# Performance work log

Hardware: AMD Instinct MI355X
Metric: run time of the kernel (lower is better)

Reference implementation:

```python
import jax, jax.numpy as jnp
import numpy as np

N_NODES = 100000
N_EDGES = 1600000
D_IN, D_HID, D_OUT = 64, 64, 32


def _glorot(key, shape):
    fan_in, fan_out = shape[0], shape[1]
    lim = np.sqrt(6.0 / (fan_in + fan_out)).astype(np.float32)
    return jax.random.uniform(key, shape, jnp.float32, -lim, lim)


def setup_inputs() -> dict:
    key = jax.random.key(0)
    ks = jax.random.split(key, 12)
    x = jax.random.normal(ks[0], (N_NODES, D_IN), jnp.float32)
    edge_index = jax.random.randint(ks[1], (2, N_EDGES), 0, N_NODES, jnp.int64)
    return {
        "x": x,
        "edge_index": edge_index,
        # SAGEConv 1 (in->hid): lin_l (aggregated neighbors, with bias), lin_r (root, no bias)
        "Wl1": _glorot(ks[2], (D_IN, D_HID)),
        "Wr1": _glorot(ks[3], (D_IN, D_HID)),
        "b1": jnp.zeros((D_HID,), jnp.float32),
        # SAGEConv 2 (hid->out)
        "Wl2": _glorot(ks[4], (D_HID, D_OUT)),
        "Wr2": _glorot(ks[5], (D_HID, D_OUT)),
        "b2": jnp.zeros((D_OUT,), jnp.float32),
        # trust head: Linear(32,16) -> ReLU -> Linear(16,1) -> Sigmoid (dropout inert in eval)
        "Wt1": _glorot(ks[6], (D_OUT, 16)),
        "bt1": jnp.zeros((16,), jnp.float32),
        "Wt2": _glorot(ks[7], (16, 1)),
        "bt2": jnp.zeros((1,), jnp.float32),
    }


def _sage_conv(x, src, dst, Wl, Wr, b):
    # mean-aggregate neighbor messages: msg flows src -> dst
    msg = x[src]                                              # [E, d] gather
    agg_sum = jax.ops.segment_sum(msg, dst, num_segments=N_NODES)
    deg = jax.ops.segment_sum(jnp.ones((src.shape[0],), x.dtype), dst,
                              num_segments=N_NODES)
    agg = agg_sum / jnp.maximum(deg, 1.0)[:, None]            # zero-degree -> 0
    return agg @ Wl + x @ Wr + b


def reference(x, edge_index, Wl1, Wr1, b1, Wl2, Wr2, b2, Wt1, bt1, Wt2, bt2):
    src, dst = edge_index[0], edge_index[1]
    h = _sage_conv(x, src, dst, Wl1, Wr1, b1)
    h = jax.nn.relu(h)                    # dropout p=0.3 inert in eval
    h = _sage_conv(h, src, dst, Wl2, Wr2, b2)
    t = jax.nn.relu(h @ Wt1 + bt1)        # dropout p=0.2 inert in eval
    trust = jax.nn.sigmoid(t @ Wt2 + bt2)
    return h, trust
```

## Files before the change

### kernel.cpp

```cpp
#include <hip/hip_runtime.h>
#include <math.h>


#define BCAP    9216
#define BKCHUNK 4096

__device__ inline unsigned short f2bf(float x) {
    unsigned u = __float_as_uint(x);
    unsigned r = u + 0x7fffu + ((u >> 16) & 1u);
    return (unsigned short)(r >> 16);
}
__device__ inline unsigned pack2(float a, float b) {
    return (unsigned)f2bf(a) | ((unsigned)f2bf(b) << 16);
}
__device__ inline float bflo(unsigned u) { return __uint_as_float(u << 16); }
__device__ inline float bfhi(unsigned u) { return __uint_as_float(u & 0xffff0000u); }

__global__ __launch_bounds__(256) void k_m1(
    const float* __restrict__ x,
    const float* __restrict__ Wl1, const float* __restrict__ Wr1,
    const float* __restrict__ b1,
    unsigned* __restrict__ u16b, float* __restrict__ v,
    const int* __restrict__ src, const int* __restrict__ dst,
    int* __restrict__ gcnt, unsigned* __restrict__ pairs,
    int N, int E, int nbuck, int GB)
{
    __shared__ __align__(16) char smem[50176];
    int tid = threadIdx.x;

    if ((int)blockIdx.x >= GB) {
        int* hist = (int*)smem;
        int e0 = ((int)blockIdx.x - GB) * BKCHUNK;
        int e1 = min(e0 + BKCHUNK, E);

        hist[tid] = 0;
        __syncthreads();
        for (int e = e0 + tid; e < e1; e += 256)
            atomicAdd(&hist[((unsigned)dst[e]) >> 9], 1);
        __syncthreads();
        if (tid < nbuck && hist[tid] > 0)
            hist[tid] = tid * BCAP + atomicAdd(&gcnt[tid], hist[tid]);
        __syncthreads();
        for (int e = e0 + tid; e < e1; e += 256) {
            int t = dst[e];
            int b = ((unsigned)t) >> 9;
            int pos = atomicAdd(&hist[b], 1);
            pairs[pos] = (unsigned)src[e] | ((unsigned)(t & 511) << 17);
        }
        return;
    }

    float* sXT = (float*)smem;
    float* sW  = (float*)(smem + 17408);
    int nblk = blockIdx.x * 64;

    for (int i = tid * 4; i < 64 * 64; i += 1024) {
        int r = i >> 6, c = i & 63;
        int node = nblk + r;
        float4 xv = (node < N) ? *(const float4*)&x[(size_t)node * 64 + c]
                               : make_float4(0.f, 0.f, 0.f, 0.f);
        sXT[(c + 0) * 68 + r] = xv.x;
        sXT[(c + 1) * 68 + r] = xv.y;
        sXT[(c + 2) * 68 + r] = xv.z;
        sXT[(c + 3) * 68 + r] = xv.w;
    }
    for (int i = tid * 4; i < 64 * 128; i += 1024) {
        int k = i >> 7, n = i & 127;
        const float* Wsrc = (n < 64) ? (Wl1 + k * 64 + n) : (Wr1 + k * 64 + (n - 64));
        *(float4*)&sW[k * 128 + n] = *(const float4*)Wsrc;
    }
    __syncthreads();

    int mg = tid >> 4, ng = tid & 15;
    int m0 = mg * 4, n0 = ng * 8;

    float acc[4][8];
    #pragma unroll
    for (int mi = 0; mi < 4; ++mi)
        #pragma unroll
        for (int ni = 0; ni < 8; ++ni) acc[mi][ni] = 0.0f;

    #pragma unroll 8
    for (int k = 0; k < 64; ++k) {
        float4 a  = *(float4*)&sXT[k * 68 + m0];
        float4 w0 = *(float4*)&sW[k * 128 + n0];
        float4 w1 = *(float4*)&sW[k * 128 + n0 + 4];
        float av[4] = {a.x, a.y, a.z, a.w};
        float wv[8] = {w0.x, w0.y, w0.z, w0.w, w1.x, w1.y, w1.z, w1.w};
        #pragma unroll
        for (int mi = 0; mi < 4; ++mi)
            #pragma unroll
            for (int ni = 0; ni < 8; ++ni)
                acc[mi][ni] = fmaf(av[mi], wv[ni], acc[mi][ni]);
    }

    bool isV = (n0 >= 64);
    if (isV) {
        float4 b0 = *(const float4*)&b1[n0 - 64];
        float4 b4 = *(const float4*)&b1[n0 - 64 + 4];
        float bb[8] = {b0.x, b0.y, b0.z, b0.w, b4.x, b4.y, b4.z, b4.w};
        #pragma unroll
        for (int mi = 0; mi < 4; ++mi) {
            int node = nblk + m0 + mi;
            if (node >= N) continue;
            float* dstp = &v[(size_t)node * 64 + (n0 - 64)];
            *(float4*)&dstp[0] = make_float4(acc[mi][0]+bb[0], acc[mi][1]+bb[1],
                                             acc[mi][2]+bb[2], acc[mi][3]+bb[3]);
            *(float4*)&dstp[4] = make_float4(acc[mi][4]+bb[4], acc[mi][5]+bb[5],
                                             acc[mi][6]+bb[6], acc[mi][7]+bb[7]);
        }
    } else {
        #pragma unroll
        for (int mi = 0; mi < 4; ++mi) {
            int node = nblk + m0 + mi;
            if (node >= N) continue;
            uint4 pk;
            pk.x = pack2(acc[mi][0], acc[mi][1]);
            pk.y = pack2(acc[mi][2], acc[mi][3]);
            pk.z = pack2(acc[mi][4], acc[mi][5]);
            pk.w = pack2(acc[mi][6], acc[mi][7]);
            *(uint4*)&u16b[(size_t)node * 32 + (n0 >> 1)] = pk;
        }
    }
}

__global__ __launch_bounds__(512) void k_csr(
    const unsigned* __restrict__ pairs, const int* __restrict__ gcnt,
    int2* __restrict__ nodeOff, int* __restrict__ adj, int N)
{
    __shared__ int hist[512];
    __shared__ int waveSum[8];
    int b = blockIdx.x;
    int tid = threadIdx.x;
    int count = min(gcnt[b], BCAP);
    const unsigned* pp = pairs + (size_t)b * BCAP;
    int base = b * BCAP;

    hist[tid] = 0;
    __syncthreads();
    for (int j = tid; j < count; j += 512)
        atomicAdd(&hist[pp[j] >> 17], 1);
    __syncthreads();

    int deg = hist[tid];
    int lane = tid & 63, wid = tid >> 6;
    int incl = deg;
    #pragma unroll
    for (int off = 1; off < 64; off <<= 1) {
        int t = __shfl_up(incl, off);
        if (lane >= off) incl += t;
    }
    if (lane == 63) waveSum[wid] = incl;
    __syncthreads();
    if (wid == 0 && lane < 8) {
        int s = waveSum[lane], orig = s;
        #pragma unroll
        for (int off = 1; off < 8; off <<= 1) {
            int t = __shfl_up(s, off);
            if (lane >= off) s += t;
        }
        waveSum[lane] = s - orig;
    }
    __syncthreads();
    int excl = incl - deg + waveSum[wid];

    int node = b * 512 + tid;
    if (node < N) nodeOff[node] = make_int2(base + excl, deg);
    __syncthreads();
    hist[tid] = excl;
    __syncthreads();

    for (int j = tid; j < count; j += 512) {
        unsigned e = pp[j];
        int pos = atomicAdd(&hist[e >> 17], 1);
        adj[base + pos] = (int)(e & 0x1FFFFu);
    }
}

__global__ __launch_bounds__(512) void k_m2(
    const int2* __restrict__ nodeOff, const int* __restrict__ adj,
    const unsigned* __restrict__ u16b, const float* __restrict__ v,
    const float* __restrict__ Wl2, const float* __restrict__ Wr2,
    const float* __restrict__ b2,
    unsigned* __restrict__ P16b, float* __restrict__ Qout, int N)
{
    __shared__ float sH[64 * 66];
    __shared__ float sW[64 * 64];
    int tid = threadIdx.x;
    int nodeBase = blockIdx.x * 64;

    for (int i = tid * 4; i < 64 * 64; i += 2048) {
        int k = i >> 6, n = i & 63;
        const float* Wsrc = (n < 32) ? (Wl2 + k * 32 + n) : (Wr2 + k * 32 + (n - 32));
        *(float4*)&sW[k * 64 + n] = *(const float4*)Wsrc;
    }

    int hw = tid >> 5;
    int lane = tid & 31;
    #pragma unroll
    for (int r = 0; r < 4; ++r) {
        int nLoc = hw * 4 + r;
        int n = nodeBase + nLoc;
        float h0 = 0.0f, h1v = 0.0f;
        if (n < N) {
            int2 od = nodeOff[n];
            int beg = od.x, end = od.x + od.y;
            float lo0=0.f,hi0=0.f,lo1=0.f,hi1=0.f,lo2=0.f,hi2=0.f,lo3=0.f,hi3=0.f;
            int i = beg;
            for (; i + 4 <= end; i += 4) {
                int s0 = adj[i], s1 = adj[i+1], s2 = adj[i+2], s3 = adj[i+3];
                unsigned w0 = u16b[(size_t)s0 * 32 + lane];
                unsigned w1 = u16b[(size_t)s1 * 32 + lane];
                unsigned w2 = u16b[(size_t)s2 * 32 + lane];
                unsigned w3 = u16b[(size_t)s3 * 32 + lane];
                lo0 += bflo(w0); hi0 += bfhi(w0);
                lo1 += bflo(w1); hi1 += bfhi(w1);
                lo2 += bflo(w2); hi2 += bfhi(w2);
                lo3 += bflo(w3); hi3 += bfhi(w3);
            }
            for (; i < end; ++i) {
                unsigned w = u16b[(size_t)adj[i] * 32 + lane];
                lo0 += bflo(w); hi0 += bfhi(w);
            }
            float mlo = (lo0 + lo1) + (lo2 + lo3);
            float mhi = (hi0 + hi1) + (hi2 + hi3);
            float invd = (od.y > 0) ? 1.0f / (float)od.y : 1.0f;
            float2 vv = ((const float2*)v)[(size_t)n * 32 + lane];
            h0  = fmaxf(mlo * invd + vv.x, 0.0f);
            h1v = fmaxf(mhi * invd + vv.y, 0.0f);
        }
        *(float2*)&sH[nLoc * 66 + 2 * lane] = make_float2(h0, h1v);
    }
    __syncthreads();

    int ng = tid & 15;
    int mg = tid >> 4;
    int m0 = mg * 2, n0 = ng * 4;

    float acc[2][4];
    #pragma unroll
    for (int mi = 0; mi < 2; ++mi)
        #pragma unroll
        for (int ni = 0; ni < 4; ++ni) acc[mi][ni] = 0.0f;

    #pragma unroll 8
    for (int k = 0; k < 64; ++k) {
        float a0 = sH[(m0 + 0) * 66 + k];
        float a1 = sH[(m0 + 1) * 66 + k];
        float4 w = *(float4*)&sW[k * 64 + n0];
        float wv[4] = {w.x, w.y, w.z, w.w};
        #pragma unroll
        for (int ni = 0; ni < 4; ++ni) {
            acc[0][ni] = fmaf(a0, wv[ni], acc[0][ni]);
            acc[1][ni] = fmaf(a1, wv[ni], acc[1][ni]);
        }
    }

    if (n0 < 32) {
        #pragma unroll
        for (int mi = 0; mi < 2; ++mi) {
            int node = nodeBase + m0 + mi;
            if (node >= N) continue;
            uint2 pk;
            pk.x = pack2(acc[mi][0], acc[mi][1]);
            pk.y = pack2(acc[mi][2], acc[mi][3]);
            *(uint2*)&P16b[(size_t)node * 16 + (n0 >> 1)] = pk;
        }
    } else {
        float4 b0 = *(const float4*)&b2[n0 - 32];
        #pragma unroll
        for (int mi = 0; mi < 2; ++mi) {
            int node = nodeBase + m0 + mi;
            if (node >= N) continue;
            *(float4*)&Qout[(size_t)node * 32 + (n0 - 32)] =
                make_float4(acc[mi][0]+b0.x, acc[mi][1]+b0.y,
                            acc[mi][2]+b0.z, acc[mi][3]+b0.w);
        }
    }
}

__global__ __launch_bounds__(256) void k_agg2(
    const int2* __restrict__ nodeOff, const int* __restrict__ adj,
    const unsigned* __restrict__ P16b, const float* __restrict__ Q,
    const float* __restrict__ Wt1, const float* __restrict__ bt1,
    const float* __restrict__ Wt2, const float* __restrict__ bt2,
    float* __restrict__ out_h, float* __restrict__ out_trust, int N)
{
    __shared__ float sWt1[32 * 16];
    __shared__ float sWt2[16];
    for (int i = threadIdx.x; i < 512; i += 256) sWt1[i] = Wt1[i];
    if (threadIdx.x < 16) sWt2[threadIdx.x] = Wt2[threadIdx.x];
    __syncthreads();

    int n = blockIdx.x * 16 + (threadIdx.x >> 4);
    int lane = threadIdx.x & 15;
    if (n >= N) return;

    int2 od = nodeOff[n];
    int beg = od.x, end = od.x + od.y;
    float lo0=0.f,hi0=0.f,lo1=0.f,hi1=0.f,lo2=0.f,hi2=0.f,lo3=0.f,hi3=0.f;
    int i = beg;
    for (; i + 4 <= end; i += 4) {
        int s0 = adj[i], s1 = adj[i+1], s2 = adj[i+2], s3 = adj[i+3];
        unsigned w0 = P16b[(size_t)s0 * 16 + lane];
        unsigned w1 = P16b[(size_t)s1 * 16 + lane];
        unsigned w2 = P16b[(size_t)s2 * 16 + lane];
        unsigned w3 = P16b[(size_t)s3 * 16 + lane];
        lo0 += bflo(w0); hi0 += bfhi(w0);
        lo1 += bflo(w1); hi1 += bfhi(w1);
        lo2 += bflo(w2); hi2 += bfhi(w2);
        lo3 += bflo(w3); hi3 += bfhi(w3);
    }
    for (; i < end; ++i) {
        unsigned w = P16b[(size_t)adj[i] * 16 + lane];
        lo0 += bflo(w); hi0 += bfhi(w);
    }
    float invd = (od.y > 0) ? 1.0f / (float)od.y : 1.0f;
    float2 qv = ((const float2*)Q)[(size_t)n * 16 + lane];
    float hx = ((lo0 + lo1) + (lo2 + lo3)) * invd + qv.x;
    float hy = ((hi0 + hi1) + (hi2 + hi3)) * invd + qv.y;

    ((float2*)out_h)[(size_t)n * 16 + lane] = make_float2(hx, hy);

    float t = bt1[lane];
    #pragma unroll
    for (int k = 0; k < 16; ++k) {
        float hlo = __shfl(hx, k, 16);
        float hhi = __shfl(hy, k, 16);
        t += hlo * sWt1[(2 * k) * 16 + lane] + hhi * sWt1[(2 * k + 1) * 16 + lane];
    }
    t = fmaxf(t, 0.0f);
    float z = t * sWt2[lane];
    z += __shfl_xor(z, 1);
    z += __shfl_xor(z, 2);
    z += __shfl_xor(z, 4);
    z += __shfl_xor(z, 8);
    if (lane == 0) out_trust[n] = 1.0f / (1.0f + expf(-(z + bt2[0])));
}


extern "C" void kernel_launch(void* const* d_in, const int* in_sizes, int n_in,
                              void* d_out, int out_size, void* d_ws, size_t ws_size,
                              hipStream_t stream)
{
    const float* x   = (const float*)d_in[0];
    const int*   ei  = (const int*)d_in[1];
    const float* Wl1 = (const float*)d_in[2];
    const float* Wr1 = (const float*)d_in[3];
    const float* b1  = (const float*)d_in[4];
    const float* Wl2 = (const float*)d_in[5];
    const float* Wr2 = (const float*)d_in[6];
    const float* b2  = (const float*)d_in[7];
    const float* Wt1 = (const float*)d_in[8];
    const float* bt1 = (const float*)d_in[9];
    const float* Wt2 = (const float*)d_in[10];
    const float* bt2 = (const float*)d_in[11];

    const int N = in_sizes[0] / 64;
    const int E = in_sizes[1] / 2;
    const int* src = ei;
    const int* dst = ei + E;
    const int nbuck = (N + 511) / 512;

    unsigned* pairs  = (unsigned*)d_ws;
    unsigned* u16b   = pairs + (size_t)nbuck * BCAP;
    float*    v      = (float*)(u16b + (size_t)N * 32);
    unsigned* P16b   = (unsigned*)(v + (size_t)N * 64);
    float*    Q      = (float*)(P16b + (size_t)N * 16);
    int*      gcnt   = (int*)(Q + (size_t)N * 32);
    int2*     nodeOff= (int2*)(gcnt + 256);
    int*      adj    = (int*)(nodeOff + N);

    hipMemsetAsync(gcnt, 0, 256 * sizeof(int), stream);

    const int GB  = (N + 63) / 64;
    const int BKB = (E + BKCHUNK - 1) / BKCHUNK;
    k_m1  <<<GB + BKB, 256, 0, stream>>>(x, Wl1, Wr1, b1, u16b, v,
                                         src, dst, gcnt, pairs, N, E, nbuck, GB);
    k_csr <<<nbuck, 512, 0, stream>>>(pairs, gcnt, nodeOff, adj, N);
    k_m2  <<<GB, 512, 0, stream>>>(nodeOff, adj, u16b, v, Wl2, Wr2, b2,
                                   P16b, Q, N);

    float* out_h     = (float*)d_out;
    float* out_trust = out_h + (size_t)N * 32;
    k_agg2<<<(N + 15) / 16, 256, 0, stream>>>(nodeOff, adj, P16b, Q,
                                              Wt1, bt1, Wt2, bt2,
                                              out_h, out_trust, N);
}
```

Baseline: 248.9 us.

## Interleave bucketing blocks with GEMM tiles, split layer-1 GEMM into two passes, widen gathers

The first kernel now interleaves one edge-bucketing block for every four GEMM tile blocks, so the atomic-heavy bucketing work is spread across the grid instead of trailing the GEMM blocks. The layer-1 GEMM computes Wl1 and Wr1 in two sequential passes with a 64x64 weight tile in shared memory, which shrinks the LDS footprint and accumulator registers so more blocks can be resident, at the cost of reloading the x tile's products and an extra barrier. The CSR build kernel runs 1024 threads per block so each bucket's edges are processed by more threads. Both aggregation kernels unroll the neighbor gather to 8 independent loads and accumulators to raise memory-level parallelism, at some register cost.

Result: no change. 246.9 us (-0.8%).

```diff
diff --git a/kernel.cpp b/kernel.cpp
--- a/kernel.cpp
+++ b/kernel.cpp
@@ -23,14 +23,16 @@
     unsigned* __restrict__ u16b, float* __restrict__ v,
     const int* __restrict__ src, const int* __restrict__ dst,
     int* __restrict__ gcnt, unsigned* __restrict__ pairs,
-    int N, int E, int nbuck, int GB)
-{
-    __shared__ __align__(16) char smem[50176];
+    int N, int E, int nbuck, int GB, int BKB)
+{
+    __shared__ __align__(16) char smem[33792];
     int tid = threadIdx.x;
-
-    if ((int)blockIdx.x >= GB) {
+    int g = blockIdx.x / 5, r5 = blockIdx.x % 5;
+
+    if (r5 == 4) {
+        if (g >= BKB) return;
         int* hist = (int*)smem;
-        int e0 = ((int)blockIdx.x - GB) * BKCHUNK;
+        int e0 = g * BKCHUNK;
         int e1 = min(e0 + BKCHUNK, E);
 
         hist[tid] = 0;
@@ -50,9 +52,11 @@
         return;
     }
 
+    int tile = 4 * g + r5;
+    if (tile >= GB) return;
     float* sXT = (float*)smem;
     float* sW  = (float*)(smem + 17408);
-    int nblk = blockIdx.x * 64;
+    int nblk = tile * 64;
 
     for (int i = tid * 4; i < 64 * 64; i += 1024) {
         int r = i >> 6, c = i & 63;
@@ -64,67 +68,62 @@
         sXT[(c + 2) * 68 + r] = xv.z;
         sXT[(c + 3) * 68 + r] = xv.w;
     }
-    for (int i = tid * 4; i < 64 * 128; i += 1024) {
-        int k = i >> 7, n = i & 127;
-        const float* Wsrc = (n < 64) ? (Wl1 + k * 64 + n) : (Wr1 + k * 64 + (n - 64));
-        *(float4*)&sW[k * 128 + n] = *(const float4*)Wsrc;
-    }
-    __syncthreads();
 
     int mg = tid >> 4, ng = tid & 15;
-    int m0 = mg * 4, n0 = ng * 8;
-
-    float acc[4][8];
+    int m0 = mg * 4, n0 = ng * 4;
+
     #pragma unroll
-    for (int mi = 0; mi < 4; ++mi)
-        #pragma unroll
-        for (int ni = 0; ni < 8; ++ni) acc[mi][ni] = 0.0f;
-
-    #pragma unroll 8
-    for (int k = 0; k < 64; ++k) {
-        float4 a  = *(float4*)&sXT[k * 68 + m0];
-        float4 w0 = *(float4*)&sW[k * 128 + n0];
-        float4 w1 = *(float4*)&sW[k * 128 + n0 + 4];
-        float av[4] = {a.x, a.y, a.z, a.w};
-        float wv[8] = {w0.x, w0.y, w0.z, w0.w, w1.x, w1.y, w1.z, w1.w};
+    for (int pass = 0; pass < 2; ++pass) {
+        const float* W = pass ? Wr1 : Wl1;
+        if (pass) __syncthreads();
+        for (int i = tid * 4; i < 64 * 64; i += 1024)
+            *(float4*)&sW[i] = *(const float4*)&W[i];
+        __syncthreads();
+
+        float acc[4][4];
         #pragma unroll
         for (int mi = 0; mi < 4; ++mi)
             #pragma unroll
-            for (int ni = 0; ni < 8; ++ni)
-                acc[mi][ni] = fmaf(av[mi], wv[ni], acc[mi][ni]);
-    }
-
-    bool isV = (n0 >= 64);
-    if (isV) {
-        float4 b0 = *(const float4*)&b1[n0 - 64];
-        float4 b4 = *(const float4*)&b1[n0 - 64 + 4];
-        float bb[8] = {b0.x, b0.y, b0.z, b0.w, b4.x, b4.y, b4.z, b4.w};
-        #pragma unroll
-        for (int mi = 0; mi < 4; ++mi) {
-            int node = nblk + m0 + mi;
-            if (node >= N) continue;
-            float* dstp = &v[(size_t)node * 64 + (n0 - 64)];
-            *(float4*)&dstp[0] = make_float4(acc[mi][0]+bb[0], acc[mi][1]+bb[1],
-                                             acc[mi][2]+bb[2], acc[mi][3]+bb[3]);
-            *(float4*)&dstp[4] = make_float4(acc[mi][4]+bb[4], acc[mi][5]+bb[5],
-                                             acc[mi][6]+bb[6], acc[mi][7]+bb[7]);
-        }
-    } else {
-        #pragma unroll
-        for (int mi = 0; mi < 4; ++mi) {
-            int node = nblk + m0 + mi;
-            if (node >= N) continue;
-            uint4 pk;
-            pk.x = pack2(acc[mi][0], acc[mi][1]);
-            pk.y = pack2(acc[mi][2], acc[mi][3]);
-            pk.z = pack2(acc[mi][4], acc[mi][5]);
-            pk.w = pack2(acc[mi][6], acc[mi][7]);
-            *(uint4*)&u16b[(size_t)node * 32 + (n0 >> 1)] = pk;
-        }
-    }
-}
-
-__global__ __launch_bounds__(512) void k_csr(
+            for (int ni = 0; ni < 4; ++ni) acc[mi][ni] = 0.0f;
+
+        #pragma unroll 8
+        for (int k = 0; k < 64; ++k) {
+            float4 a = *(float4*)&sXT[k * 68 + m0];
+            float4 w = *(float4*)&sW[k * 64 + n0];
+            float av[4] = {a.x, a.y, a.z, a.w};
+            float wv[4] = {w.x, w.y, w.z, w.w};
+            #pragma unroll
+            for (int mi = 0; mi < 4; ++mi)
+                #pragma unroll
+                for (int ni = 0; ni < 4; ++ni)
+                    acc[mi][ni] = fmaf(av[mi], wv[ni], acc[mi][ni]);
+        }
+
+        if (pass == 0) {
+            #pragma unroll
+            for (int mi = 0; mi < 4; ++mi) {
+                int node = nblk + m0 + mi;
+                if (node >= N) continue;
+                uint2 pk;
+                pk.x = pack2(acc[mi][0], acc[mi][1]);
+                pk.y = pack2(acc[mi][2], acc[mi][3]);
+                *(uint2*)&u16b[(size_t)node * 32 + (n0 >> 1)] = pk;
+            }
+        } else {
+            float4 b0 = *(const float4*)&b1[n0];
+            #pragma unroll
+            for (int mi = 0; mi < 4; ++mi) {
+                int node = nblk + m0 + mi;
+                if (node >= N) continue;
+                *(float4*)&v[(size_t)node * 64 + n0] =
+                    make_float4(acc[mi][0]+b0.x, acc[mi][1]+b0.y,
+                                acc[mi][2]+b0.z, acc[mi][3]+b0.w);
+            }
+        }
+    }
+}
+
+__global__ __launch_bounds__(1024) void k_csr(
     const unsigned* __restrict__ pairs, const int* __restrict__ gcnt,
     int2* __restrict__ nodeOff, int* __restrict__ adj, int N)
 {
@@ -136,21 +135,24 @@
     const unsigned* pp = pairs + (size_t)b * BCAP;
     int base = b * BCAP;
 
-    hist[tid] = 0;
-    __syncthreads();
-    for (int j = tid; j < count; j += 512)
+    if (tid < 512) hist[tid] = 0;
+    __syncthreads();
+    for (int j = tid; j < count; j += 1024)
         atomicAdd(&hist[pp[j] >> 17], 1);
     __syncthreads();
 
-    int deg = hist[tid];
     int lane = tid & 63, wid = tid >> 6;
-    int incl = deg;
-    #pragma unroll
-    for (int off = 1; off < 64; off <<= 1) {
-        int t = __shfl_up(incl, off);
-        if (lane >= off) incl += t;
-    }
-    if (lane == 63) waveSum[wid] = incl;
+    int deg = 0, incl = 0;
+    if (tid < 512) {
+        deg = hist[tid];
+        incl = deg;
+        #pragma unroll
+        for (int off = 1; off < 64; off <<= 1) {
+            int t = __shfl_up(incl, off);
+            if (lane >= off) incl += t;
+        }
+        if (lane == 63) waveSum[wid] = incl;
+    }
     __syncthreads();
     if (wid == 0 && lane < 8) {
         int s = waveSum[lane], orig = s;
@@ -162,15 +164,17 @@
         waveSum[lane] = s - orig;
     }
     __syncthreads();
-    int excl = incl - deg + waveSum[wid];
-
-    int node = b * 512 + tid;
-    if (node < N) nodeOff[node] = make_int2(base + excl, deg);
-    __syncthreads();
-    hist[tid] = excl;
-    __syncthreads();
-
-    for (int j = tid; j < count; j += 512) {
+    int excl = 0;
+    if (tid < 512) {
+        excl = incl - deg + waveSum[wid];
+        int node = b * 512 + tid;
+        if (node < N) nodeOff[node] = make_int2(base + excl, deg);
+    }
+    __syncthreads();
+    if (tid < 512) hist[tid] = excl;
+    __syncthreads();
+
+    for (int j = tid; j < count; j += 1024) {
         unsigned e = pp[j];
         int pos = atomicAdd(&hist[e >> 17], 1);
         adj[base + pos] = (int)(e & 0x1FFFFu);
@@ -197,7 +201,6 @@
 
     int hw = tid >> 5;
     int lane = tid & 31;
-    #pragma unroll
     for (int r = 0; r < 4; ++r) {
         int nLoc = hw * 4 + r;
         int n = nodeBase + nLoc;
@@ -205,25 +208,24 @@
         if (n < N) {
             int2 od = nodeOff[n];
             int beg = od.x, end = od.x + od.y;
-            float lo0=0.f,hi0=0.f,lo1=0.f,hi1=0.f,lo2=0.f,hi2=0.f,lo3=0.f,hi3=0.f;
+            float lo[8] = {0,0,0,0,0,0,0,0}, hi[8] = {0,0,0,0,0,0,0,0};
             int i = beg;
-            for (; i + 4 <= end; i += 4) {
-                int s0 = adj[i], s1 = adj[i+1], s2 = adj[i+2], s3 = adj[i+3];
-                unsigned w0 = u16b[(size_t)s0 * 32 + lane];
-                unsigned w1 = u16b[(size_t)s1 * 32 + lane];
-                unsigned w2 = u16b[(size_t)s2 * 32 + lane];
-                unsigned w3 = u16b[(size_t)s3 * 32 + lane];
-                lo0 += bflo(w0); hi0 += bfhi(w0);
-                lo1 += bflo(w1); hi1 += bfhi(w1);
-                lo2 += bflo(w2); hi2 += bfhi(w2);
-                lo3 += bflo(w3); hi3 += bfhi(w3);
+            for (; i + 8 <= end; i += 8) {
+                int s[8];
+                #pragma unroll
+                for (int j = 0; j < 8; ++j) s[j] = adj[i + j];
+                #pragma unroll
+                for (int j = 0; j < 8; ++j) {
+                    unsigned w = u16b[(size_t)s[j] * 32 + lane];
+                    lo[j] += bflo(w); hi[j] += bfhi(w);
+                }
             }
             for (; i < end; ++i) {
                 unsigned w = u16b[(size_t)adj[i] * 32 + lane];
-                lo0 += bflo(w); hi0 += bfhi(w);
+                lo[0] += bflo(w); hi[0] += bfhi(w);
             }
-            float mlo = (lo0 + lo1) + (lo2 + lo3);
-            float mhi = (hi0 + hi1) + (hi2 + hi3);
+            float mlo = ((lo[0]+lo[1])+(lo[2]+lo[3])) + ((lo[4]+lo[5])+(lo[6]+lo[7]));
+            float mhi = ((hi[0]+hi[1])+(hi[2]+hi[3])) + ((hi[4]+hi[5])+(hi[6]+hi[7]));
             float invd = (od.y > 0) ? 1.0f / (float)od.y : 1.0f;
             float2 vv = ((const float2*)v)[(size_t)n * 32 + lane];
             h0  = fmaxf(mlo * invd + vv.x, 0.0f);
@@ -298,27 +300,29 @@
 
     int2 od = nodeOff[n];
     int beg = od.x, end = od.x + od.y;
-    float lo0=0.f,hi0=0.f,lo1=0.f,hi1=0.f,lo2=0.f,hi2=0.f,lo3=0.f,hi3=0.f;
+    float lo[8] = {0,0,0,0,0,0,0,0}, hi[8] = {0,0,0,0,0,0,0,0};
     int i = beg;
-    for (; i + 4 <= end; i += 4) {
-        int s0 = adj[i], s1 = adj[i+1], s2 = adj[i+2], s3 = adj[i+3];
-        unsigned w0 = P16b[(size_t)s0 * 16 + lane];
-        unsigned w1 = P16b[(size_t)s1 * 16 + lane];
-        unsigned w2 = P16b[(size_t)s2 * 16 + lane];
-        unsigned w3 = P16b[(size_t)s3 * 16 + lane];
-        lo0 += bflo(w0); hi0 += bfhi(w0);
-        lo1 += bflo(w1); hi1 += bfhi(w1);
-        lo2 += bflo(w2); hi2 += bfhi(w2);
-        lo3 += bflo(w3); hi3 += bfhi(w3);
+    for (; i + 8 <= end; i += 8) {
+        int s[8];
+        #pragma unroll
+        for (int j = 0; j < 8; ++j) s[j] = adj[i + j];
+        #pragma unroll
+        for (int j = 0; j < 8; ++j) {
+            unsigned w = P16b[(size_t)s[j] * 16 + lane];
+            lo[j] += bflo(w); hi[j] += bfhi(w);
+        }
     }
     for (; i < end; ++i) {
         unsigned w = P16b[(size_t)adj[i] * 16 + lane];
-        lo0 += bflo(w); hi0 += bfhi(w);
+        lo[0] += bflo(w); hi[0] += bfhi(w);
     }
     float invd = (od.y > 0) ? 1.0f / (float)od.y : 1.0f;
+    float mlo = (((lo[0]+lo[1])+(lo[2]+lo[3])) + ((lo[4]+lo[5])+(lo[6]+lo[7]))) * invd;
+    float mhi = (((hi[0]+hi[1])+(hi[2]+hi[3])) + ((hi[4]+hi[5])+(hi[6]+hi[7]))) * invd;
+
     float2 qv = ((const float2*)Q)[(size_t)n * 16 + lane];
-    float hx = ((lo0 + lo1) + (lo2 + lo3)) * invd + qv.x;
-    float hy = ((hi0 + hi1) + (hi2 + hi3)) * invd + qv.y;
+    float hx = mlo + qv.x;
+    float hy = mhi + qv.y;
 
     ((float2*)out_h)[(size_t)n * 16 + lane] = make_float2(hx, hy);
 
@@ -375,9 +379,10 @@
 
     const int GB  = (N + 63) / 64;
     const int BKB = (E + BKCHUNK - 1) / BKCHUNK;
-    k_m1  <<<GB + BKB, 256, 0, stream>>>(x, Wl1, Wr1, b1, u16b, v,
-                                         src, dst, gcnt, pairs, N, E, nbuck, GB);
-    k_csr <<<nbuck, 512, 0, stream>>>(pairs, gcnt, nodeOff, adj, N);
+    int grp = max(BKB, (GB + 3) / 4);
+    k_m1  <<<5 * grp, 256, 0, stream>>>(x, Wl1, Wr1, b1, u16b, v,
+                                        src, dst, gcnt, pairs, N, E, nbuck, GB, BKB);
+    k_csr <<<nbuck, 1024, 0, stream>>>(pairs, gcnt, nodeOff, adj, N);
     k_m2  <<<GB, 512, 0, stream>>>(nodeOff, adj, u16b, v, Wl2, Wr2, b2,
                                    P16b, Q, N);
 
```
